# Performance work log

Hardware: AMD Instinct MI355X
Metric: run time of the kernel (lower is better)

The kernel has to match this reference:

```python
import jax, jax.numpy as jnp
import numpy as np

LN_EPS = 1e-5

def _layernorm(x, g, b):
    mu = jnp.mean(x, axis=-1, keepdims=True)
    var = jnp.var(x, axis=-1, keepdims=True)
    return (x - mu) * jax.lax.rsqrt(var + LN_EPS) * g + b

def setup_inputs() -> dict:
    key = jax.random.key(0)
    ks = jax.random.split(key, 8)
    B, L, d_atom, d_hid = 8, 128, 256, 32
    return {
        "z":    jax.random.normal(ks[0], (B, L, d_atom), dtype=jnp.float32),
        "W_in": jax.random.normal(ks[1], (d_atom, 2 * d_hid), dtype=jnp.float32) * 0.02,
        "b_in": jnp.zeros((2 * d_hid,), dtype=jnp.float32),
        "ln_g": jnp.ones((2 * d_hid,), dtype=jnp.float32),
        "ln_b": jnp.zeros((2 * d_hid,), dtype=jnp.float32),
        "W1":   jax.random.normal(ks[2], (d_hid * d_hid, 21), dtype=jnp.float32) * 0.02,
        "b1":   jnp.zeros((21,), dtype=jnp.float32),
        "W2":   jax.random.normal(ks[3], (d_hid * d_hid, 30), dtype=jnp.float32) * 0.02,
        "b2":   jnp.zeros((30,), dtype=jnp.float32),
    }

def reference(z, W_in, b_in, ln_g, ln_b, W1, b1, W2, b2):
    # linear_in: Linear -> exact GELU -> LayerNorm
    ab = _layernorm(jax.nn.gelu(z @ W_in + b_in, approximate=False), ln_g, ln_b)
    h = ab.shape[-1] // 2
    a, b = ab[..., :h], ab[..., h:]              # (B, L, h) each
    # Fused bilinear form: outer(a_l, b_m) flattened to h*h, then Linear.
    # Equivalent to materializing (B, L, L, h*h) and matmul, reassociated.
    W1r = W1.reshape(h, h, -1)                   # (h, h, 21)
    W2r = W2.reshape(h, h, -1)                   # (h, h, 30)
    x1 = jnp.einsum('blc,bmd,cdk->blmk', a, b, W1r) + b1  # (B, L, L, 21)
    x2 = jnp.einsum('blc,bmd,cdk->blmk', a, b, W2r) + b2  # (B, L, L, 30)
    return (x1, x2)
```

## Files before the change

### kernel.cpp

```cpp
#include <hip/hip_runtime.h>
#include <hip/hip_bf16.h>
#include <math.h>

#define NB 8
#define NL 128
#define D_ATOM 256
#define DH 32
#define DAB 64
#define K1 21
#define K2 30
#define KT 51
#define ROWS (NB*NL)
#define LN_EPS 1e-5f

#define OUT1_ROW (NL*K1)
#define OUT2_ROW (NL*K2)
#define STAGE_N  (OUT1_ROW + OUT2_ROW)
#define WCAT 1632

typedef __attribute__((ext_vector_type(8))) short bf16x8;
typedef __attribute__((ext_vector_type(4))) float f32x4;

__device__ __forceinline__ unsigned short f2bf(float x) {
    __hip_bfloat16 h = __float2bfloat16(x);
    return *reinterpret_cast<unsigned short*>(&h);
}

__global__ __launch_bounds__(256) void ln_wprep_kernel(
    const float* __restrict__ z, const float* __restrict__ W_in,
    const float* __restrict__ b_in, const float* __restrict__ ln_g,
    const float* __restrict__ ln_b, const float* __restrict__ W1,
    const float* __restrict__ W2, float* __restrict__ a_ws,
    unsigned short* __restrict__ bbf, unsigned short* __restrict__ Wlin2)
{
    __shared__ float Wl[D_ATOM * DAB];
    __shared__ float zl[4][D_ATOM];
    const int t = threadIdx.x;
    const int w = t >> 6, j = t & 63;
    const int row0 = blockIdx.x * 4;

    #pragma unroll
    for (int s = 0; s < 16; ++s) {
        int i4 = t + s * 256;
        ((float4*)Wl)[i4] = ((const float4*)W_in)[i4];
    }
    ((float4*)zl)[t] = ((const float4*)(z + (size_t)row0 * D_ATOM))[t];
    __syncthreads();

    float acc = b_in[j];
    #pragma unroll 8
    for (int i = 0; i < D_ATOM; ++i)
        acc = fmaf(zl[w][i], Wl[i * DAB + j], acc);

    float g = 0.5f * acc * (1.0f + erff(acc * 0.70710678118654752f));

    float s = g, sq = g * g;
    #pragma unroll
    for (int msk = 1; msk < 64; msk <<= 1) {
        s  += __shfl_xor(s,  msk, 64);
        sq += __shfl_xor(sq, msk, 64);
    }
    float mu  = s  * (1.0f / 64.0f);
    float var = sq * (1.0f / 64.0f) - mu * mu;
    float y = (g - mu) * rsqrtf(var + LN_EPS) * ln_g[j] + ln_b[j];

    const int row = row0 + w;
    if (j < DH) {
        a_ws[row * DH + j] = y;
    } else {
        const int d = j - DH, m = row & 127, batch = row >> 7;
        bbf[batch * 4096 + ((m >> 4) << 9) +
            ((((m & 15) | ((d >> 3) << 4)) << 3) | (d & 7))] = f2bf(y);
    }

    if (t < 32) {
        int p  = (int)blockIdx.x * 32 + t;
        int c  = p >> 8, t2 = p & 255;
        unsigned short v[8];
        #pragma unroll
        for (int s2 = 0; s2 < 8; ++s2) {
            int o = s2 * 256 + t2;
            float val = 0.f;
            if (o < 672)       val = W1[c * 672 + o];
            else if (o < WCAT) val = W2[c * 960 + (o - 672)];
            v[s2] = f2bf(val);
        }
        uint4 wq;
        wq.x = (unsigned)v[0] | ((unsigned)v[1] << 16);
        wq.y = (unsigned)v[2] | ((unsigned)v[3] << 16);
        wq.z = (unsigned)v[4] | ((unsigned)v[5] << 16);
        wq.w = (unsigned)v[6] | ((unsigned)v[7] << 16);
        ((uint4*)Wlin2)[p] = wq;
    }
}

__global__ __launch_bounds__(256, 4) void pair_kernel(
    const float* __restrict__ a_ws, const unsigned short* __restrict__ bbf,
    const unsigned short* __restrict__ Wlin2, const float* __restrict__ b1v,
    const float* __restrict__ b2v, float* __restrict__ out)
{
    const int row0  = blockIdx.x * 2;
    const int batch = row0 >> 7;
    const int t     = threadIdx.x;
    const int w  = t >> 6, l = t & 63;
    const int lg = l >> 4, li = l & 15;

    __shared__ unsigned short Tf[2 * 4 * 64 * 8];
    __shared__ __align__(16) float stg[STAGE_N];
    __shared__ float al[2][DH];

    #pragma unroll
    for (int s = 0; s < 8; ++s)
        ((unsigned int*)Tf)[t + s * 256] = 0u;
    if (t < 2 * DH) al[t >> 5][t & 31] = a_ws[row0 * DH + t];
    __syncthreads();

    {
        float tacc0[7], tacc1[7];
        int fidx[7];
        bool val[7];
        #pragma unroll
        for (int s = 0; s < 7; ++s) {
            int o = t + s * 256;
            val[s] = (o < WCAT);
            int oo = val[s] ? o : 0;
            int d, k;
            if (oo < 672) { d = oo / 21; k = oo % 21; }
            else { int o2 = oo - 672; d = o2 / 30; k = 21 + o2 % 30; }
            fidx[s] = (((k >> 4) * 64 + ((k & 15) | ((d >> 3) << 4))) << 3) | (d & 7);
            tacc0[s] = 0.f; tacc1[s] = 0.f;
        }
        const uint4* wbase = ((const uint4*)Wlin2) + t;
        #pragma unroll 4
        for (int c = 0; c < DH; ++c) {
            float ac0 = al[0][c], ac1 = al[1][c];
            uint4 wq = wbase[c * 256];
            float wv[7];
            wv[0] = __uint_as_float(wq.x << 16);
            wv[1] = __uint_as_float(wq.x & 0xffff0000u);
            wv[2] = __uint_as_float(wq.y << 16);
            wv[3] = __uint_as_float(wq.y & 0xffff0000u);
            wv[4] = __uint_as_float(wq.z << 16);
            wv[5] = __uint_as_float(wq.z & 0xffff0000u);
            wv[6] = __uint_as_float(wq.w << 16);
            #pragma unroll
            for (int s = 0; s < 7; ++s) {
                tacc0[s] = fmaf(ac0, wv[s], tacc0[s]);
                tacc1[s] = fmaf(ac1, wv[s], tacc1[s]);
            }
        }
        #pragma unroll
        for (int s = 0; s < 7; ++s) {
            if (val[s]) {
                Tf[fidx[s]]        = f2bf(tacc0[s]);
                Tf[2048 + fidx[s]] = f2bf(tacc1[s]);
            }
        }
    }
    __syncthreads();

    const int r  = w >> 1;
    const int mh = w & 1;

    bf16x8 afr[4], bfr[4];
    #pragma unroll
    for (int i = 0; i < 4; ++i)
        afr[i] = ((const bf16x8*)bbf)[batch * 512 + (mh * 4 + i) * 64 + l];
    #pragma unroll
    for (int kt = 0; kt < 4; ++kt)
        bfr[kt] = ((const bf16x8*)Tf)[(r * 4 + kt) * 64 + l];

    float bias[4];
    #pragma unroll
    for (int kt = 0; kt < 4; ++kt) {
        int k = kt * 16 + li;
        bias[kt] = (k < K1) ? b1v[k] : (k < KT ? b2v[k - K1] : 0.f);
    }

    #pragma unroll
    for (int rr = 0; rr < 2; ++rr) {
        if (r == rr) {
            #pragma unroll
            for (int i = 0; i < 4; ++i) {
                const int mbase = (mh * 4 + i) * 16 + lg * 4;
                #pragma unroll
                for (int kt = 0; kt < 4; ++kt) {
                    f32x4 acc = __builtin_amdgcn_mfma_f32_16x16x32_bf16(
                        afr[i], bfr[kt], (f32x4){0.f, 0.f, 0.f, 0.f}, 0, 0, 0);
                    const int k = kt * 16 + li;
                    if (k < K1) {
                        #pragma unroll
                        for (int q = 0; q < 4; ++q)
                            stg[(mbase + q) * K1 + k] = acc[q] + bias[kt];
                    } else if (k < KT) {
                        #pragma unroll
                        for (int q = 0; q < 4; ++q)
                            stg[OUT1_ROW + (mbase + q) * K2 + (k - K1)] = acc[q] + bias[kt];
                    }
                }
            }
        }
        __syncthreads();

        const int row = row0 + rr;
        float* o1 = out + (size_t)row * OUT1_ROW;
        float* o2 = out + (size_t)ROWS * OUT1_ROW + (size_t)row * OUT2_ROW;
        const float4* s1 = (const float4*)stg;
        const float4* s2 = (const float4*)(stg + OUT1_ROW);
        for (int i4 = t; i4 < OUT1_ROW / 4; i4 += 256)
            ((float4*)o1)[i4] = s1[i4];
        for (int i4 = t; i4 < OUT2_ROW / 4; i4 += 256)
            ((float4*)o2)[i4] = s2[i4];
        if (rr == 0) __syncthreads();
    }
}

extern "C" void kernel_launch(void* const* d_in, const int* in_sizes, int n_in,
                              void* d_out, int out_size, void* d_ws, size_t ws_size,
                              hipStream_t stream) {
    const float* z    = (const float*)d_in[0];
    const float* W_in = (const float*)d_in[1];
    const float* b_in = (const float*)d_in[2];
    const float* ln_g = (const float*)d_in[3];
    const float* ln_b = (const float*)d_in[4];
    const float* W1   = (const float*)d_in[5];
    const float* b1   = (const float*)d_in[6];
    const float* W2   = (const float*)d_in[7];
    const float* b2   = (const float*)d_in[8];
    float* out = (float*)d_out;

    float*          a_ws  = (float*)d_ws;
    unsigned short* bbf   = (unsigned short*)(a_ws + 32768);
    unsigned short* Wlin2 = bbf + 32768;

    ln_wprep_kernel<<<256, 256, 0, stream>>>(z, W_in, b_in, ln_g, ln_b,
                                             W1, W2, a_ws, bbf, Wlin2);
    pair_kernel<<<ROWS / 2, 256, 0, stream>>>(a_ws, bbf, Wlin2, b1, b2, out);
}
```

Measured before the change: 22.94 us.

## Register-tile input projection with split-K reduction through shared memory

Replaces the per-thread 256-long serial dot product in the first kernel with a split-K scheme. Each thread computes a 4-row by 4-column register tile over a 16-element K chunk using float4 LDS loads, then the 16 partial sums are reduced through a shared buffer. This cuts LDS traffic per FMA and shortens the serial dependency chain. In exchange it adds an extra shared array, another barrier and a reduction pass.

```diff
diff --git a/kernel.cpp b/kernel.cpp
--- a/kernel.cpp
+++ b/kernel.cpp
@@ -34,9 +34,12 @@
     unsigned short* __restrict__ bbf, unsigned short* __restrict__ Wlin2)
 {
     __shared__ float Wl[D_ATOM * DAB];
-    __shared__ float zl[4][D_ATOM];
+    __shared__ float zT[D_ATOM][4];
+    __shared__ float red[16][4][DAB];
+
     const int t = threadIdx.x;
-    const int w = t >> 6, j = t & 63;
+    const int w = t >> 6, l = t & 63;
+    const int g = l >> 4, c4 = l & 15;
     const int row0 = blockIdx.x * 4;
 
     #pragma unroll
@@ -44,17 +47,50 @@
         int i4 = t + s * 256;
         ((float4*)Wl)[i4] = ((const float4*)W_in)[i4];
     }
-    ((float4*)zl)[t] = ((const float4*)(z + (size_t)row0 * D_ATOM))[t];
-    __syncthreads();
-
-    float acc = b_in[j];
-    #pragma unroll 8
-    for (int i = 0; i < D_ATOM; ++i)
-        acc = fmaf(zl[w][i], Wl[i * DAB + j], acc);
-
-    float g = 0.5f * acc * (1.0f + erff(acc * 0.70710678118654752f));
-
-    float s = g, sq = g * g;
+    {
+        float4 v = ((const float4*)(z + (size_t)row0 * D_ATOM))[t];
+        int r = t >> 6, i0 = (t & 63) * 4;
+        zT[i0 + 0][r] = v.x; zT[i0 + 1][r] = v.y;
+        zT[i0 + 2][r] = v.z; zT[i0 + 3][r] = v.w;
+    }
+    __syncthreads();
+
+    float acc[4][4];
+    #pragma unroll
+    for (int r = 0; r < 4; ++r)
+        #pragma unroll
+        for (int q = 0; q < 4; ++q) acc[r][q] = 0.f;
+
+    const int ibase = w * 64 + g * 16;
+    #pragma unroll
+    for (int it = 0; it < 16; ++it) {
+        const int i = ibase + it;
+        float4 wv = *(const float4*)&Wl[i * DAB + 4 * c4];
+        float4 zv = *(const float4*)&zT[i][0];
+        float zr[4] = {zv.x, zv.y, zv.z, zv.w};
+        float wq[4] = {wv.x, wv.y, wv.z, wv.w};
+        #pragma unroll
+        for (int r = 0; r < 4; ++r)
+            #pragma unroll
+            for (int q = 0; q < 4; ++q)
+                acc[r][q] = fmaf(zr[r], wq[q], acc[r][q]);
+    }
+    const int p = w * 4 + g;
+    #pragma unroll
+    for (int r = 0; r < 4; ++r) {
+        float4 v = {acc[r][0], acc[r][1], acc[r][2], acc[r][3]};
+        *(float4*)&red[p][r][4 * c4] = v;
+    }
+    __syncthreads();
+
+    const int j = l;
+    float a2 = b_in[j];
+    #pragma unroll
+    for (int pp = 0; pp < 16; ++pp) a2 += red[pp][w][j];
+
+    float gg = 0.5f * a2 * (1.0f + erff(a2 * 0.70710678118654752f));
+
+    float s = gg, sq = gg * gg;
     #pragma unroll
     for (int msk = 1; msk < 64; msk <<= 1) {
         s  += __shfl_xor(s,  msk, 64);
@@ -62,7 +98,7 @@
     }
     float mu  = s  * (1.0f / 64.0f);
     float var = sq * (1.0f / 64.0f) - mu * mu;
-    float y = (g - mu) * rsqrtf(var + LN_EPS) * ln_g[j] + ln_b[j];
+    float y = (gg - mu) * rsqrtf(var + LN_EPS) * ln_g[j] + ln_b[j];
 
     const int row = row0 + w;
     if (j < DH) {
@@ -74,8 +110,8 @@
     }
 
     if (t < 32) {
-        int p  = (int)blockIdx.x * 32 + t;
-        int c  = p >> 8, t2 = p & 255;
+        int pw = (int)blockIdx.x * 32 + t;
+        int c  = pw >> 8, t2 = pw & 255;
         unsigned short v[8];
         #pragma unroll
         for (int s2 = 0; s2 < 8; ++s2) {
@@ -90,7 +126,7 @@
         wq.y = (unsigned)v[2] | ((unsigned)v[3] << 16);
         wq.z = (unsigned)v[4] | ((unsigned)v[5] << 16);
         wq.w = (unsigned)v[6] | ((unsigned)v[7] << 16);
-        ((uint4*)Wlin2)[p] = wq;
+        ((uint4*)Wlin2)[pw] = wq;
     }
 }
 
```

Measured after the change: 21.51 us. 1.07x faster.
